# Optimization experiments

Hardware: AMD Instinct MI355X
Metric: run time of the kernel (lower is better)

## Reference

```python
import jax, jax.numpy as jnp
import numpy as np

OUT = 56          # roi_align / mask resolution
SCALE = 0.25      # spatial_scale (bases at stride 4)
CO = 14           # raw coefficient resolution


def _roi_align_one(feat, box):
    """torchvision roi_align, aligned=True, sampling_ratio=1.
    feat: [B, H, W] base maps for this roi's image; box: [4] = (x0,y0,x1,y1).
    Returns [B, OUT, OUT]."""
    H, W = feat.shape[1], feat.shape[2]
    s = box * SCALE - 0.5  # aligned=True half-pixel offset
    x0, y0, x1, y1 = s[0], s[1], s[2], s[3]
    bw = (x1 - x0) / OUT
    bh = (y1 - y0) / OUT
    # sampling_ratio=1 -> single sample at each bin center
    xs = x0 + (jnp.arange(OUT, dtype=feat.dtype) + 0.5) * bw
    ys = y0 + (jnp.arange(OUT, dtype=feat.dtype) + 0.5) * bh
    vy = (ys >= -1.0) & (ys <= H)
    vx = (xs >= -1.0) & (xs <= W)
    yc = jnp.clip(ys, 0.0, H - 1)
    xc = jnp.clip(xs, 0.0, W - 1)
    yl = jnp.clip(jnp.floor(yc).astype(jnp.int32), 0, H - 2); yh = yl + 1
    xl = jnp.clip(jnp.floor(xc).astype(jnp.int32), 0, W - 2); xh = xl + 1
    ly = yc - yl; hy = 1.0 - ly
    lx = xc - xl; hx = 1.0 - lx
    fll = feat[:, yl, :][:, :, xl]; flh = feat[:, yl, :][:, :, xh]
    fhl = feat[:, yh, :][:, :, xl]; fhh = feat[:, yh, :][:, :, xh]
    val = (hy[:, None] * (hx[None, :] * fll + lx[None, :] * flh)
           + ly[:, None] * (hx[None, :] * fhl + lx[None, :] * fhh))
    return val * (vy[:, None] & vx[None, :])


def _paste_masks(masks, boxes, img_h, img_w):
    """do_paste_mask: grid_sample(bilinear, align_corners=False, zero pad).
    The grid is separable (y depends on row, x on column), so express it as two
    batched matmuls with tent-kernel weights. masks: [N,56,56] -> [N,img_h,img_w]."""
    x0, y0, x1, y1 = (boxes[:, 0:1], boxes[:, 1:2], boxes[:, 2:3], boxes[:, 3:4])
    gy = ((jnp.arange(img_h, dtype=masks.dtype) + 0.5 - y0) / (y1 - y0)) * 2.0 - 1.0  # [N,H]
    gx = ((jnp.arange(img_w, dtype=masks.dtype) + 0.5 - x0) / (x1 - x0)) * 2.0 - 1.0  # [N,W]
    # unnormalize (align_corners=False): f = (g+1)*size/2 - 0.5
    fy = (gy + 1.0) * OUT * 0.5 - 0.5
    fx = (gx + 1.0) * OUT * 0.5 - 0.5
    idx = jnp.arange(OUT, dtype=masks.dtype)
    Wy = jnp.maximum(0.0, 1.0 - jnp.abs(fy[:, :, None] - idx))  # [N, img_h, 56]
    Wx = jnp.maximum(0.0, 1.0 - jnp.abs(fx[:, :, None] - idx))  # [N, img_w, 56]
    rows = jnp.einsum('nhm,nmw->nhw', Wy, masks)                # [N, img_h, 56]
    return jnp.einsum('nhw,nqw->nhq', rows, Wx)                 # [N, img_h, img_w]


def setup_inputs() -> dict:
    key = jax.random.key(0)
    ks = jax.random.split(key, 6)
    b_h, b_w = 136, 200                 # bases at stride 4 of a 544x800 image
    img_h, img_w = b_h * 4, b_w * 4
    N, Bb = 100, 4
    bases = jax.random.normal(ks[0], (1, Bb, b_h, b_w), jnp.float32)
    x0 = jax.random.uniform(ks[1], (N, 1), minval=0.0, maxval=img_w * 0.55)
    y0 = jax.random.uniform(ks[2], (N, 1), minval=0.0, maxval=img_h * 0.55)
    w = jax.random.uniform(ks[3], (N, 1), minval=32.0, maxval=img_w * 0.4)
    h = jax.random.uniform(ks[4], (N, 1), minval=32.0, maxval=img_h * 0.4)
    boxes = jnp.concatenate([x0, y0,
                             jnp.minimum(x0 + w, img_w - 1.0),
                             jnp.minimum(y0 + h, img_h - 1.0)], axis=1)
    top = jax.random.normal(ks[5], (N, Bb * CO * CO), jnp.float32)
    box_feat = jnp.concatenate([jnp.zeros((N, 1), jnp.float32), boxes, top], axis=1)
    return {"bases": bases, "box_feat": box_feat}


def reference(bases, box_feat):
    bidx = box_feat[:, 0].astype(jnp.int32)
    boxes = box_feat[:, 1:5]
    top_feat = box_feat[:, 5:]
    N = box_feat.shape[0]
    Bb, b_h, b_w = bases.shape[1], bases.shape[2], bases.shape[3]
    # roi_align over all detections
    rois = jax.vmap(lambda i, b: _roi_align_one(bases[i], b))(bidx, boxes)  # [N,B,56,56]
    # merge_bases: upsample 14->56 (bilinear, align_corners=False), softmax over bases, blend
    coeffs = top_feat.reshape(N, Bb, CO, CO)
    coeffs = jax.image.resize(coeffs, (N, Bb, OUT, OUT), method='bilinear')
    coeffs = jax.nn.softmax(coeffs, axis=1)
    masks = jax.nn.sigmoid(jnp.sum(rois * coeffs, axis=1))  # [N,56,56]
    return _paste_masks(masks, boxes, b_h * 4, b_w * 4)      # [N, 4*b_h, 4*b_w]
```

## Files before the change

### kernel.cpp

```cpp
#include <hip/hip_runtime.h>
#include <math.h>

#define OUTD 56
#define COD  14
#define BH   136
#define BW   200
#define IMGH 544
#define IMGW 800
#define BB   4
#define BFS  789

__global__ __launch_bounds__(256) void mask_kernel(
    const float* __restrict__ bases,
    const float* __restrict__ box_feat,
    float* __restrict__ masks) {
  const int n = blockIdx.y;
  const int p = blockIdx.x * 256 + threadIdx.x;
  if (p >= OUTD * OUTD) return;
  const int y = p / OUTD;
  const int x = p - y * OUTD;

  const float* bf = box_feat + (size_t)n * BFS;
  const int bidx = (int)bf[0];
  const float x0 = bf[1], y0 = bf[2], x1 = bf[3], y1 = bf[4];
  const float sx0 = x0 * 0.25f - 0.5f;
  const float sy0 = y0 * 0.25f - 0.5f;
  const float bwv = (x1 - x0) * 0.25f * (1.0f / OUTD);
  const float bhv = (y1 - y0) * 0.25f * (1.0f / OUTD);
  const float* feat = bases + (size_t)bidx * BB * BH * BW;
  const float* top  = bf + 5;

  const float ysv = sy0 + ((float)y + 0.5f) * bhv;
  const float xsv = sx0 + ((float)x + 0.5f) * bwv;
  const float valid =
      (ysv >= -1.0f && ysv <= (float)BH && xsv >= -1.0f && xsv <= (float)BW)
          ? 1.0f : 0.0f;
  const float yc = fminf(fmaxf(ysv, 0.0f), (float)(BH - 1));
  const float xc = fminf(fmaxf(xsv, 0.0f), (float)(BW - 1));
  int yl = (int)floorf(yc); yl = yl > (BH - 2) ? (BH - 2) : yl;
  int xl = (int)floorf(xc); xl = xl > (BW - 2) ? (BW - 2) : xl;
  const float ly = yc - (float)yl, hy = 1.0f - ly;
  const float lx = xc - (float)xl, hx = 1.0f - lx;
  const float w00 = hy * hx, w01 = hy * lx, w10 = ly * hx, w11 = ly * lx;

  float cyf = fminf(fmaxf(((float)y + 0.5f) * 0.25f - 0.5f, 0.0f), (float)(COD - 1));
  float cxf = fminf(fmaxf(((float)x + 0.5f) * 0.25f - 0.5f, 0.0f), (float)(COD - 1));
  int cyl = (int)floorf(cyf); cyl = cyl > (COD - 2) ? (COD - 2) : cyl;
  int cxl = (int)floorf(cxf); cxl = cxl > (COD - 2) ? (COD - 2) : cxl;
  const float cly = cyf - (float)cyl, chy = 1.0f - cly;
  const float clx = cxf - (float)cxl, chx = 1.0f - clx;
  const float cw00 = chy * chx, cw01 = chy * clx, cw10 = cly * chx, cw11 = cly * clx;

  float rvals[BB], cvals[BB];
#pragma unroll
  for (int b = 0; b < BB; ++b) {
    const float* fb = feat + b * BH * BW;
    const float r = w00 * fb[yl * BW + xl]       + w01 * fb[yl * BW + xl + 1] +
                    w10 * fb[(yl + 1) * BW + xl] + w11 * fb[(yl + 1) * BW + xl + 1];
    rvals[b] = r * valid;
    const float* tb = top + b * COD * COD;
    cvals[b] = cw00 * tb[cyl * COD + cxl]       + cw01 * tb[cyl * COD + cxl + 1] +
               cw10 * tb[(cyl + 1) * COD + cxl] + cw11 * tb[(cyl + 1) * COD + cxl + 1];
  }

  const float mx = fmaxf(fmaxf(cvals[0], cvals[1]), fmaxf(cvals[2], cvals[3]));
  float e[BB], s = 0.0f;
#pragma unroll
  for (int b = 0; b < BB; ++b) { e[b] = __expf(cvals[b] - mx); s += e[b]; }
  const float inv = 1.0f / s;
  float dot = 0.0f;
#pragma unroll
  for (int b = 0; b < BB; ++b) dot += rvals[b] * (e[b] * inv);
  masks[(size_t)n * (OUTD * OUTD) + p] = 1.0f / (1.0f + __expf(-dot));
}

__global__ __launch_bounds__(256) void paste_kernel(
    const float* __restrict__ masks,
    const float* __restrict__ box_feat,
    float4* __restrict__ out) {
  const int h = blockIdx.x;
  const int n = blockIdx.y;
  const int tid = threadIdx.x;

  const float* bf = box_feat + (size_t)n * BFS;
  const float y0 = bf[2], y1 = bf[4];
  float4* orow = out + ((size_t)n * IMGH + h) * (IMGW / 4);

  const float fy = ((float)h + 0.5f - y0) * ((float)OUTD / (y1 - y0)) - 0.5f;

  if (!(fy > -1.0f && fy < (float)OUTD)) {
    if (tid < IMGW / 4) orow[tid] = make_float4(0.f, 0.f, 0.f, 0.f);
    return;
  }

  const int ml = (int)floorf(fy);
  const float wy1 = fy - (float)ml;
  const float wy0 = 1.0f - wy1;

  __shared__ float mrow[2][OUTD];
  if (tid < 2 * OUTD) {
    const int r_idx = (tid >= OUTD) ? 1 : 0;
    const int x = tid - r_idx * OUTD;
    const int r = ml + r_idx;
    float v = 0.0f;
    if (r >= 0 && r < OUTD)
      v = masks[(size_t)n * (OUTD * OUTD) + r * OUTD + x];
    mrow[r_idx][x] = v;
  }
  __syncthreads();

  if (tid >= IMGW / 4) return;

  const float x0 = bf[1], x1 = bf[3];
  const float invw = (float)OUTD / (x1 - x0);
  const float cx = (0.5f - x0) * invw - 0.5f;

  float res[4];
#pragma unroll
  for (int i = 0; i < 4; ++i) {
    const float q = (float)(tid * 4 + i);
    const float fx = fmaf(q, invw, cx);
    float v = 0.0f;
    if (fx > -1.0f && fx < (float)OUTD) {
      const int xl = (int)floorf(fx);
      float wx1 = fx - (float)xl;
      float wx0 = 1.0f - wx1;
      const int xls = xl < 0 ? 0 : xl;
      const int xhs = (xl + 1 > OUTD - 1) ? (OUTD - 1) : (xl + 1);
      if (xl < 0) wx0 = 0.0f;
      if (xl + 1 > OUTD - 1) wx1 = 0.0f;
      v = wy0 * (wx0 * mrow[0][xls] + wx1 * mrow[0][xhs]) +
          wy1 * (wx0 * mrow[1][xls] + wx1 * mrow[1][xhs]);
    }
    res[i] = v;
  }
  orow[tid] = make_float4(res[0], res[1], res[2], res[3]);
}

extern "C" void kernel_launch(void* const* d_in, const int* in_sizes, int n_in,
                              void* d_out, int out_size, void* d_ws, size_t ws_size,
                              hipStream_t stream) {
  const float* bases    = (const float*)d_in[0];
  const float* box_feat = (const float*)d_in[1];
  const int N = in_sizes[1] / BFS;

  float* masks = (float*)d_ws;

  dim3 g1((OUTD * OUTD + 255) / 256, N);
  mask_kernel<<<g1, 256, 0, stream>>>(bases, box_feat, masks);

  dim3 g2(IMGH, N);
  paste_kernel<<<g2, 256, 0, stream>>>(masks, box_feat, (float4*)d_out);
}
```

Measured before the change: 170.9 us.

## Process 16 output rows per paste block with hoisted x weights

The paste kernel now handles 16 image rows per block instead of one. The per-column x indices and weights are computed once and reused for every row. Mask rows are read directly from global memory (cache), which drops the shared-memory staging and the barrier. This cuts launch and block overhead and repeated x-weight math for an output-write-bound kernel, at the cost of fewer blocks and uncoalesced gather loads from global instead of shared memory.

```diff
diff --git a/kernel.cpp b/kernel.cpp
--- a/kernel.cpp
+++ b/kernel.cpp
@@ -9,6 +9,7 @@
 #define IMGW 800
 #define BB   4
 #define BFS  789
+#define RPB  16
 
 __global__ __launch_bounds__(256) void mask_kernel(
     const float* __restrict__ bases,
@@ -78,63 +79,68 @@
     const float* __restrict__ masks,
     const float* __restrict__ box_feat,
     float4* __restrict__ out) {
-  const int h = blockIdx.x;
-  const int n = blockIdx.y;
+  const int n  = blockIdx.y;
+  const int h0 = blockIdx.x * RPB;
   const int tid = threadIdx.x;
+  const bool active = tid < (IMGW / 4);
 
   const float* bf = box_feat + (size_t)n * BFS;
-  const float y0 = bf[2], y1 = bf[4];
-  float4* orow = out + ((size_t)n * IMGH + h) * (IMGW / 4);
+  const float x0 = bf[1], y0 = bf[2], x1 = bf[3], y1 = bf[4];
 
-  const float fy = ((float)h + 0.5f - y0) * ((float)OUTD / (y1 - y0)) - 0.5f;
+  const float invw = (float)OUTD / (x1 - x0);
+  const float cx = (0.5f - x0) * invw - 0.5f;
+  const float invh = (float)OUTD / (y1 - y0);
+  const float cy = (0.5f - y0) * invh - 0.5f;
 
-  if (!(fy > -1.0f && fy < (float)OUTD)) {
-    if (tid < IMGW / 4) orow[tid] = make_float4(0.f, 0.f, 0.f, 0.f);
-    return;
+  int   xls[4], xhs[4];
+  float wx0[4], wx1[4];
+#pragma unroll
+  for (int i = 0; i < 4; ++i) {
+    const float q  = (float)(tid * 4 + i);
+    const float fx = fmaf(q, invw, cx);
+    const bool vx = (fx > -1.0f && fx < (float)OUTD);
+    const int xl = (int)floorf(fx);
+    float w1 = fx - (float)xl;
+    float w0 = 1.0f - w1;
+    if (xl < 0)            w0 = 0.0f;
+    if (xl + 1 > OUTD - 1) w1 = 0.0f;
+    int lo = xl     < 0        ? 0        : xl;
+    lo     = lo     > OUTD - 1 ? OUTD - 1 : lo;
+    int hi = xl + 1 < 0        ? 0        : xl + 1;
+    hi     = hi     > OUTD - 1 ? OUTD - 1 : hi;
+    xls[i] = lo;
+    xhs[i] = hi;
+    wx0[i] = vx ? w0 : 0.0f;
+    wx1[i] = vx ? w1 : 0.0f;
   }
 
-  const int ml = (int)floorf(fy);
-  const float wy1 = fy - (float)ml;
-  const float wy0 = 1.0f - wy1;
+  const float* mbase = masks + (size_t)n * (OUTD * OUTD);
+  float4* orow = out + ((size_t)n * IMGH + h0) * (IMGW / 4) + tid;
 
-  __shared__ float mrow[2][OUTD];
-  if (tid < 2 * OUTD) {
-    const int r_idx = (tid >= OUTD) ? 1 : 0;
-    const int x = tid - r_idx * OUTD;
-    const int r = ml + r_idx;
-    float v = 0.0f;
-    if (r >= 0 && r < OUTD)
-      v = masks[(size_t)n * (OUTD * OUTD) + r * OUTD + x];
-    mrow[r_idx][x] = v;
+  for (int r = 0; r < RPB; ++r) {
+    const int h = h0 + r;
+    const float fy = fmaf((float)h, invh, cy);
+    float4 v = make_float4(0.f, 0.f, 0.f, 0.f);
+    if (fy > -1.0f && fy < (float)OUTD) {
+      const int ml = (int)floorf(fy);
+      float wy1 = fy - (float)ml;
+      float wy0 = 1.0f - wy1;
+      const int r0 = ml < 0 ? 0 : ml;
+      const int r1 = (ml + 1 > OUTD - 1) ? (OUTD - 1) : (ml + 1);
+      if (ml < 0)            wy0 = 0.0f;
+      if (ml + 1 > OUTD - 1) wy1 = 0.0f;
+      const float* m0 = mbase + r0 * OUTD;
+      const float* m1 = mbase + r1 * OUTD;
+      float res[4];
+#pragma unroll
+      for (int i = 0; i < 4; ++i) {
+        res[i] = wy0 * (wx0[i] * m0[xls[i]] + wx1[i] * m0[xhs[i]]) +
+                 wy1 * (wx0[i] * m1[xls[i]] + wx1[i] * m1[xhs[i]]);
+      }
+      v = make_float4(res[0], res[1], res[2], res[3]);
+    }
+    if (active) orow[(size_t)r * (IMGW / 4)] = v;
   }
-  __syncthreads();
-
-  if (tid >= IMGW / 4) return;
-
-  const float x0 = bf[1], x1 = bf[3];
-  const float invw = (float)OUTD / (x1 - x0);
-  const float cx = (0.5f - x0) * invw - 0.5f;
-
-  float res[4];
-#pragma unroll
-  for (int i = 0; i < 4; ++i) {
-    const float q = (float)(tid * 4 + i);
-    const float fx = fmaf(q, invw, cx);
-    float v = 0.0f;
-    if (fx > -1.0f && fx < (float)OUTD) {
-      const int xl = (int)floorf(fx);
-      float wx1 = fx - (float)xl;
-      float wx0 = 1.0f - wx1;
-      const int xls = xl < 0 ? 0 : xl;
-      const int xhs = (xl + 1 > OUTD - 1) ? (OUTD - 1) : (xl + 1);
-      if (xl < 0) wx0 = 0.0f;
-      if (xl + 1 > OUTD - 1) wx1 = 0.0f;
-      v = wy0 * (wx0 * mrow[0][xls] + wx1 * mrow[0][xhs]) +
-          wy1 * (wx0 * mrow[1][xls] + wx1 * mrow[1][xhs]);
-    }
-    res[i] = v;
-  }
-  orow[tid] = make_float4(res[0], res[1], res[2], res[3]);
 }
 
 extern "C" void kernel_launch(void* const* d_in, const int* in_sizes, int n_in,
@@ -149,6 +155,6 @@
   dim3 g1((OUTD * OUTD + 255) / 256, N);
   mask_kernel<<<g1, 256, 0, stream>>>(bases, box_feat, masks);
 
-  dim3 g2(IMGH, N);
+  dim3 g2(IMGH / RPB, N);
   paste_kernel<<<g2, 256, 0, stream>>>(masks, box_feat, (float4*)d_out);
 }
```

Measured after the change: 182.6 us. +6.8%, slower.
